# Kernel optimization log

Hardware: AMD Instinct MI355X
Metric: run time of the kernel (lower is better)

Reference implementation:

```python
import jax, jax.numpy as jnp
import numpy as np

B, L, D = 32, 1024, 1024

def setup_inputs() -> dict:
    key = jax.random.key(0)
    k1, k2 = jax.random.split(key)
    x = jax.random.normal(k1, (B, L, D), dtype=jnp.float32)
    x_mask = jax.random.randint(k2, (B, L), 0, 2, dtype=jnp.int32)
    return {"x": x, "x_mask": x_mask}

def reference(x, x_mask):
    # scores: [B, L, L] = x @ x^T
    scores = jnp.einsum('bld,bmd->blm', x, x)
    # zero out the diagonal (the python loop in the original)
    L_ = x.shape[1]
    eye = jnp.eye(L_, dtype=scores.dtype)
    scores = scores * (1.0 - eye)
    # allennlp util.masked_softmax (default, non-memory-efficient form):
    #   a = softmax(scores * mask) * mask; a = a / (a.sum(-1) + 1e-13)
    mask = x_mask[:, None, :].astype(scores.dtype)  # [B, 1, L] broadcast over query dim
    a = jax.nn.softmax(scores * mask, axis=-1) * mask
    alpha = a / (jnp.sum(a, axis=-1, keepdims=True) + 1e-13)
    # matched_seq: [B, L, D]
    return jnp.einsum('blm,bmd->bld', alpha, x)
```

## Files before the change

### kernel.cpp

```cpp
#include <hip/hip_runtime.h>


typedef _Float16 half8 __attribute__((ext_vector_type(8)));
typedef float f32x4 __attribute__((ext_vector_type(4)));

#define L_ 1024
#define D_ 1024

__device__ __forceinline__ half8 cvt8(const float* src) {
  float4 a = *(const float4*)src;
  float4 c = *(const float4*)(src + 4);
  half8 h;
  h[0] = (_Float16)a.x; h[1] = (_Float16)a.y; h[2] = (_Float16)a.z; h[3] = (_Float16)a.w;
  h[4] = (_Float16)c.x; h[5] = (_Float16)c.y; h[6] = (_Float16)c.z; h[7] = (_Float16)c.w;
  return h;
}


__global__ void sam_cvt(const float* __restrict__ x, _Float16* __restrict__ xh) {
  const size_t base = ((size_t)blockIdx.x * 256 + threadIdx.x) * 32;
  const float* src = x + base;
  _Float16* dst = xh + base;
#pragma unroll
  for (int i = 0; i < 4; ++i)
    *(half8*)(dst + i * 8) = cvt8(src + i * 8);
}

__global__ __launch_bounds__(1024, 4) void sam_scores3(
    const _Float16* __restrict__ xh, const int* __restrict__ xmask,
    _Float16* __restrict__ alpha)
{
  const int qblk = blockIdx.x;
  const int b    = blockIdx.y;
  const int tid  = threadIdx.x;
  const int wave = tid >> 6;
  const int lane = tid & 63;
  const int qw   = wave >> 3;
  const int kw   = wave & 7;
  const int l15  = lane & 15;
  const int quad = lane >> 4;

  __shared__ _Float16 Qs[64][72];
  __shared__ union KsAt {
    _Float16 Ks[1024][72];
    _Float16 At[64][1032];
  } KU;
  __shared__ float rmax[8][64];
  __shared__ float rsum[8][64];

  const _Float16* xb = xh + (size_t)b * L_ * D_;
  const int srow = tid >> 3;
  const int scol = (tid & 7) * 8;

  f32x4 acc[2][8];
#pragma unroll
  for (int m = 0; m < 2; ++m)
#pragma unroll
    for (int n = 0; n < 8; ++n)
#pragma unroll
      for (int r = 0; r < 4; ++r) acc[m][n][r] = 0.0f;

  for (int dc = 0; dc < 16; ++dc) {
    if (tid < 512)
      *(half8*)&Qs[srow][scol] =
          *(const half8*)(xb + (size_t)(qblk * 64 + srow) * D_ + dc * 64 + scol);
#pragma unroll
    for (int i = 0; i < 8; ++i)
      *(half8*)&KU.Ks[srow + 128 * i][scol] =
          *(const half8*)(xb + (size_t)(srow + 128 * i) * D_ + dc * 64 + scol);
    __syncthreads();
#pragma unroll
    for (int ks = 0; ks < 2; ++ks) {
      half8 af[2], bf[8];
#pragma unroll
      for (int m = 0; m < 2; ++m)
        af[m] = *(half8*)&Qs[qw * 32 + 16 * m + l15][ks * 32 + quad * 8];
#pragma unroll
      for (int n = 0; n < 8; ++n)
        bf[n] = *(half8*)&KU.Ks[kw * 128 + 16 * n + l15][ks * 32 + quad * 8];
#pragma unroll
      for (int m = 0; m < 2; ++m)
#pragma unroll
        for (int n = 0; n < 8; ++n)
          acc[m][n] = __builtin_amdgcn_mfma_f32_16x16x32_f16(af[m], bf[n], acc[m][n], 0, 0, 0);
    }
    __syncthreads();
  }

  float mkv[8];
#pragma unroll
  for (int n = 0; n < 8; ++n)
    mkv[n] = (float)xmask[b * L_ + kw * 128 + 16 * n + l15];

  float rst[2][4];
#pragma unroll
  for (int m = 0; m < 2; ++m)
#pragma unroll
    for (int r = 0; r < 4; ++r) rst[m][r] = 0.0f;

#pragma unroll
  for (int m = 0; m < 2; ++m)
#pragma unroll
    for (int r = 0; r < 4; ++r) {
      const int gq = qblk * 64 + qw * 32 + 16 * m + quad * 4 + r;
#pragma unroll
      for (int n = 0; n < 8; ++n) {
        const int gk = kw * 128 + 16 * n + l15;
        float v = acc[m][n][r];
        if (gq == gk) v = 0.0f;
        v = (mkv[n] != 0.0f) ? v : 0.0f;
        acc[m][n][r] = v;
        rst[m][r] = fmaxf(rst[m][r], v);
      }
    }
#pragma unroll
  for (int m = 0; m < 2; ++m)
#pragma unroll
    for (int r = 0; r < 4; ++r) {
      float v = rst[m][r];
      v = fmaxf(v, __shfl_xor(v, 1));
      v = fmaxf(v, __shfl_xor(v, 2));
      v = fmaxf(v, __shfl_xor(v, 4));
      v = fmaxf(v, __shfl_xor(v, 8));
      rst[m][r] = v;
    }
  if (l15 == 0) {
#pragma unroll
    for (int m = 0; m < 2; ++m)
#pragma unroll
      for (int r = 0; r < 4; ++r)
        rmax[kw][qw * 32 + 16 * m + quad * 4 + r] = rst[m][r];
  }
  __syncthreads();

  float Mrow[2][4];
#pragma unroll
  for (int m = 0; m < 2; ++m)
#pragma unroll
    for (int r = 0; r < 4; ++r) {
      const int row = qw * 32 + 16 * m + quad * 4 + r;
      float M = fmaxf(fmaxf(rmax[0][row], rmax[1][row]), fmaxf(rmax[2][row], rmax[3][row]));
      M = fmaxf(M, fmaxf(fmaxf(rmax[4][row], rmax[5][row]), fmaxf(rmax[6][row], rmax[7][row])));
      Mrow[m][r] = M;
      rst[m][r] = 0.0f;
    }
#pragma unroll
  for (int m = 0; m < 2; ++m)
#pragma unroll
    for (int r = 0; r < 4; ++r)
#pragma unroll
      for (int n = 0; n < 8; ++n) {
        float w = (mkv[n] != 0.0f) ? __expf(acc[m][n][r] - Mrow[m][r]) : 0.0f;
        acc[m][n][r] = w;
        rst[m][r] += w;
      }
#pragma unroll
  for (int m = 0; m < 2; ++m)
#pragma unroll
    for (int r = 0; r < 4; ++r) {
      float v = rst[m][r];
      v += __shfl_xor(v, 1);
      v += __shfl_xor(v, 2);
      v += __shfl_xor(v, 4);
      v += __shfl_xor(v, 8);
      rst[m][r] = v;
    }
  if (l15 == 0) {
#pragma unroll
    for (int m = 0; m < 2; ++m)
#pragma unroll
      for (int r = 0; r < 4; ++r)
        rsum[kw][qw * 32 + 16 * m + quad * 4 + r] = rst[m][r];
  }
  __syncthreads();

#pragma unroll
  for (int m = 0; m < 2; ++m)
#pragma unroll
    for (int r = 0; r < 4; ++r) {
      const int row = qw * 32 + 16 * m + quad * 4 + r;
      float S = rsum[0][row] + rsum[1][row] + rsum[2][row] + rsum[3][row] +
                rsum[4][row] + rsum[5][row] + rsum[6][row] + rsum[7][row];
      const float inv = 1.0f / (S + 1e-13f);
#pragma unroll
      for (int n = 0; n < 8; ++n)
        KU.At[row][kw * 128 + 16 * n + l15] = (_Float16)(acc[m][n][r] * inv);
    }
  __syncthreads();

  {
    const int orow = tid >> 4;
    const int oc   = (tid & 15) * 8;
    _Float16* gp = alpha + ((size_t)(b * L_ + qblk * 64 + orow)) * L_;
#pragma unroll
    for (int p = 0; p < 8; ++p)
      *(half8*)(gp + oc + p * 128) = *(half8*)&KU.At[orow][oc + p * 128];
  }
}

__global__ __launch_bounds__(512, 3) void sam_pv2(
    const _Float16* __restrict__ xh, const _Float16* __restrict__ alpha,
    float* __restrict__ out)
{
  const int qb   = blockIdx.x >> 1;
  const int dh   = blockIdx.x & 1;
  const int b    = blockIdx.y;
  const int tid  = threadIdx.x;
  const int wave = tid >> 6;
  const int lane = tid & 63;
  const int qw   = wave >> 2;
  const int dw   = wave & 3;
  const int l15  = lane & 15;
  const int quad = lane >> 4;

  __shared__ _Float16 Vs[512][40];
  __shared__ _Float16 As[64][40];

  f32x4 acc[2][8];
#pragma unroll
  for (int m = 0; m < 2; ++m)
#pragma unroll
    for (int n = 0; n < 8; ++n)
#pragma unroll
      for (int r = 0; r < 4; ++r) acc[m][n][r] = 0.0f;

  const int d0 = (tid & 255) * 2;
  const int kh = tid >> 8;

  for (int kc = 0; kc < 32; ++kc) {
    if (tid < 256) {
      const int ar = tid >> 2, ac = tid & 3;
      *(half8*)&As[ar][ac * 8] =
          *(const half8*)(alpha + ((size_t)(b * L_ + qb * 64 + ar)) * L_ + kc * 32 + ac * 8);
    }
    {
      const _Float16* vp = xh + ((size_t)(b * L_ + kc * 32 + kh * 16)) * D_ + dh * 512 + d0;
      half8 a0, a1, c0, c1;
#pragma unroll
      for (int kk = 0; kk < 8; ++kk) {
        union { unsigned int u; _Float16 h[2]; } cv;
        cv.u = *(const unsigned int*)(vp + (size_t)kk * D_);
        a0[kk] = cv.h[0]; c0[kk] = cv.h[1];
      }
#pragma unroll
      for (int kk = 0; kk < 8; ++kk) {
        union { unsigned int u; _Float16 h[2]; } cv;
        cv.u = *(const unsigned int*)(vp + (size_t)(kk + 8) * D_);
        a1[kk] = cv.h[0]; c1[kk] = cv.h[1];
      }
      *(half8*)&Vs[d0    ][kh * 16    ] = a0;
      *(half8*)&Vs[d0    ][kh * 16 + 8] = a1;
      *(half8*)&Vs[d0 + 1][kh * 16    ] = c0;
      *(half8*)&Vs[d0 + 1][kh * 16 + 8] = c1;
    }
    __syncthreads();
    half8 af[2], bf[8];
#pragma unroll
    for (int m = 0; m < 2; ++m)
      af[m] = *(half8*)&As[qw * 32 + 16 * m + l15][quad * 8];
#pragma unroll
    for (int n = 0; n < 8; ++n)
      bf[n] = *(half8*)&Vs[dw * 128 + 16 * n + l15][quad * 8];
#pragma unroll
    for (int m = 0; m < 2; ++m)
#pragma unroll
      for (int n = 0; n < 8; ++n)
        acc[m][n] = __builtin_amdgcn_mfma_f32_16x16x32_f16(af[m], bf[n], acc[m][n], 0, 0, 0);
    __syncthreads();
  }

#pragma unroll
  for (int m = 0; m < 2; ++m)
#pragma unroll
    for (int r = 0; r < 4; ++r) {
      const int gq = qb * 64 + qw * 32 + 16 * m + quad * 4 + r;
      float* op = out + (size_t)(b * L_ + gq) * D_ + dh * 512 + dw * 128;
#pragma unroll
      for (int n = 0; n < 8; ++n) op[16 * n + l15] = acc[m][n][r];
    }
}


__global__ __launch_bounds__(256, 2) void sam_scores_softmax(
    const float* __restrict__ x, const int* __restrict__ xmask,
    float* __restrict__ out)
{
  const int qblk = blockIdx.x;
  const int b    = blockIdx.y;
  const int tid  = threadIdx.x;
  const int wave = tid >> 6;
  const int lane = tid & 63;
  const int qh   = wave >> 1;
  const int kh   = wave & 1;
  const int l15  = lane & 15;
  const int quad = lane >> 4;

  __shared__ _Float16 Qs[128][72];
  __shared__ _Float16 Ks[256][72];
  __shared__ float msk[256];
  __shared__ float tmax[2][128];
  __shared__ float tsum[2][128];
  __shared__ float mrun[128];
  __shared__ float lrun[128];
  __shared__ float mtile[4][128];

  if (tid < 128) { mrun[tid] = 0.0f; lrun[tid] = 0.0f; }

  const float* xb = x + (size_t)b * L_ * D_;

  for (int kt = 0; kt < 4; ++kt) {
    msk[tid] = (float)xmask[b * L_ + kt * 256 + tid];

    f32x4 acc[4][8];
#pragma unroll
    for (int m = 0; m < 4; ++m)
#pragma unroll
      for (int n = 0; n < 8; ++n)
#pragma unroll
        for (int r = 0; r < 4; ++r) acc[m][n][r] = 0.0f;

    for (int dc = 0; dc < 16; ++dc) {
      {
        const int row = tid >> 1, cb = (tid & 1) * 32;
        const float* src = xb + (size_t)(qblk * 128 + row) * D_ + dc * 64 + cb;
#pragma unroll
        for (int i = 0; i < 4; ++i)
          *(half8*)&Qs[row][cb + i * 8] = cvt8(src + i * 8);
      }
      {
        const float* src = xb + (size_t)(kt * 256 + tid) * D_ + dc * 64;
#pragma unroll
        for (int i = 0; i < 8; ++i)
          *(half8*)&Ks[tid][i * 8] = cvt8(src + i * 8);
      }
      __syncthreads();
#pragma unroll
      for (int ks = 0; ks < 2; ++ks) {
        half8 af[4], bf[8];
#pragma unroll
        for (int m = 0; m < 4; ++m)
          af[m] = *(half8*)&Qs[qh * 64 + 16 * m + l15][ks * 32 + quad * 8];
#pragma unroll
        for (int n = 0; n < 8; ++n)
          bf[n] = *(half8*)&Ks[kh * 128 + 16 * n + l15][ks * 32 + quad * 8];
#pragma unroll
        for (int m = 0; m < 4; ++m)
#pragma unroll
          for (int n = 0; n < 8; ++n)
            acc[m][n] = __builtin_amdgcn_mfma_f32_16x16x32_f16(af[m], bf[n], acc[m][n], 0, 0, 0);
      }
      __syncthreads();
    }

    float mkv[8];
#pragma unroll
    for (int n = 0; n < 8; ++n) mkv[n] = msk[kh * 128 + 16 * n + l15];

    float rstat[4][4];
#pragma unroll
    for (int m = 0; m < 4; ++m)
#pragma unroll
      for (int r = 0; r < 4; ++r) rstat[m][r] = 0.0f;

#pragma unroll
    for (int m = 0; m < 4; ++m)
#pragma unroll
      for (int r = 0; r < 4; ++r) {
        const int gq = qblk * 128 + qh * 64 + 16 * m + quad * 4 + r;
#pragma unroll
        for (int n = 0; n < 8; ++n) {
          const int gk = kt * 256 + kh * 128 + 16 * n + l15;
          float v = acc[m][n][r];
          if (gq == gk) v = 0.0f;
          v = (mkv[n] != 0.0f) ? v : 0.0f;
          acc[m][n][r] = v;
          rstat[m][r] = fmaxf(rstat[m][r], v);
        }
      }
#pragma unroll
    for (int m = 0; m < 4; ++m)
#pragma unroll
      for (int r = 0; r < 4; ++r) {
        float v = rstat[m][r];
        v = fmaxf(v, __shfl_xor(v, 1));
        v = fmaxf(v, __shfl_xor(v, 2));
        v = fmaxf(v, __shfl_xor(v, 4));
        v = fmaxf(v, __shfl_xor(v, 8));
        rstat[m][r] = v;
      }
    if (l15 == 0) {
#pragma unroll
      for (int m = 0; m < 4; ++m)
#pragma unroll
        for (int r = 0; r < 4; ++r)
          tmax[kh][qh * 64 + 16 * m + quad * 4 + r] = rstat[m][r];
    }
    __syncthreads();

    float mnew[4][4];
#pragma unroll
    for (int m = 0; m < 4; ++m)
#pragma unroll
      for (int r = 0; r < 4; ++r) {
        const int row = qh * 64 + 16 * m + quad * 4 + r;
        mnew[m][r] = fmaxf(mrun[row], fmaxf(tmax[0][row], tmax[1][row]));
        rstat[m][r] = 0.0f;
      }
#pragma unroll
    for (int m = 0; m < 4; ++m)
#pragma unroll
      for (int r = 0; r < 4; ++r)
#pragma unroll
        for (int n = 0; n < 8; ++n) {
          float w = (mkv[n] != 0.0f) ? __expf(acc[m][n][r] - mnew[m][r]) : 0.0f;
          acc[m][n][r] = w;
          rstat[m][r] += w;
        }
#pragma unroll
    for (int m = 0; m < 4; ++m)
#pragma unroll
      for (int r = 0; r < 4; ++r) {
        float v = rstat[m][r];
        v += __shfl_xor(v, 1);
        v += __shfl_xor(v, 2);
        v += __shfl_xor(v, 4);
        v += __shfl_xor(v, 8);
        rstat[m][r] = v;
      }
    if (l15 == 0) {
#pragma unroll
      for (int m = 0; m < 4; ++m)
#pragma unroll
        for (int r = 0; r < 4; ++r)
          tsum[kh][qh * 64 + 16 * m + quad * 4 + r] = rstat[m][r];
    }
    __syncthreads();

    if (kh == 0 && l15 == 0) {
#pragma unroll
      for (int m = 0; m < 4; ++m)
#pragma unroll
        for (int r = 0; r < 4; ++r) {
          const int row = qh * 64 + 16 * m + quad * 4 + r;
          const float mo = mrun[row];
          const float mn = mnew[m][r];
          lrun[row] = lrun[row] * __expf(mo - mn) + tsum[0][row] + tsum[1][row];
          mrun[row] = mn;
          mtile[kt][row] = mn;
        }
    }
#pragma unroll
    for (int m = 0; m < 4; ++m)
#pragma unroll
      for (int r = 0; r < 4; ++r) {
        const int gq = qblk * 128 + qh * 64 + 16 * m + quad * 4 + r;
        _Float16* wp = (_Float16*)((char*)out + (size_t)(b * L_ + gq) * (D_ * 4));
#pragma unroll
        for (int n = 0; n < 8; ++n)
          wp[kt * 256 + kh * 128 + 16 * n + l15] = (_Float16)acc[m][n][r];
      }
    __syncthreads();
  }

  __threadfence();
  __syncthreads();
  {
    const int row = tid >> 1, hf = tid & 1;
    const int gq = qblk * 128 + row;
    char* rowp = (char*)out + (size_t)(b * L_ + gq) * (D_ * 4);
    const float Mv  = mrun[row];
    const float inv = 1.0f / (lrun[row] + 1e-13f);
    const float sc0 = __expf(mtile[hf * 2    ][row] - Mv) * inv;
    const float sc1 = __expf(mtile[hf * 2 + 1][row] - Mv) * inv;
    for (int i = 0; i < 64; ++i) {
      const int col = hf * 512 + i * 8;
      const float s = (i < 32) ? sc0 : sc1;
      half8 v = *(half8*)(rowp + col * 2);
#pragma unroll
      for (int j = 0; j < 8; ++j) v[j] = (_Float16)((float)v[j] * s);
      *(half8*)(rowp + col * 2) = v;
      *(half8*)(rowp + 2048 + col * 2) = v;
    }
  }
}

__global__ __launch_bounds__(512, 2) void sam_pv(
    const float* __restrict__ x, float* __restrict__ out)
{
  const int q128 = blockIdx.x >> 1;
  const int dh   = blockIdx.x & 1;
  const int b    = blockIdx.y;
  const int tid  = threadIdx.x;
  const int wave = tid >> 6;
  const int lane = tid & 63;
  const int qh   = wave >> 2;
  const int dq   = wave & 3;
  const int l15  = lane & 15;
  const int quad = lane >> 4;

  __shared__ _Float16 Vs[512][40];
  __shared__ _Float16 As[128][40];

  f32x4 acc[4][8];
#pragma unroll
  for (int m = 0; m < 4; ++m)
#pragma unroll
    for (int n = 0; n < 8; ++n)
#pragma unroll
      for (int r = 0; r < 4; ++r) acc[m][n][r] = 0.0f;

  const int arow  = tid >> 2, aoct = tid & 3;
  const int d0    = (tid & 255) * 2;
  const int khalf = tid >> 8;

  for (int kc = 0; kc < 32; ++kc) {
    *(half8*)&As[arow][aoct * 8] =
        *(const half8*)((const char*)out +
                        (size_t)(b * L_ + q128 * 128 + arow) * (D_ * 4) +
                        dh * 2048 + kc * 64 + aoct * 16);
    {
      const float* vs = x + (size_t)(b * L_ + kc * 32 + khalf * 16) * D_ + dh * 512 + d0;
      half8 a0, a1, c0, c1;
#pragma unroll
      for (int kk = 0; kk < 8; ++kk) {
        float2 v = *(const float2*)(vs + (size_t)kk * D_);
        a0[kk] = (_Float16)v.x; c0[kk] = (_Float16)v.y;
      }
#pragma unroll
      for (int kk = 0; kk < 8; ++kk) {
        float2 v = *(const float2*)(vs + (size_t)(kk + 8) * D_);
        a1[kk] = (_Float16)v.x; c1[kk] = (_Float16)v.y;
      }
      *(half8*)&Vs[d0    ][khalf * 16    ] = a0;
      *(half8*)&Vs[d0    ][khalf * 16 + 8] = a1;
      *(half8*)&Vs[d0 + 1][khalf * 16    ] = c0;
      *(half8*)&Vs[d0 + 1][khalf * 16 + 8] = c1;
    }
    __syncthreads();
    half8 af[4], bf[8];
#pragma unroll
    for (int m = 0; m < 4; ++m)
      af[m] = *(half8*)&As[qh * 64 + 16 * m + l15][quad * 8];
#pragma unroll
    for (int n = 0; n < 8; ++n)
      bf[n] = *(half8*)&Vs[dq * 128 + 16 * n + l15][quad * 8];
#pragma unroll
    for (int m = 0; m < 4; ++m)
#pragma unroll
      for (int n = 0; n < 8; ++n)
        acc[m][n] = __builtin_amdgcn_mfma_f32_16x16x32_f16(af[m], bf[n], acc[m][n], 0, 0, 0);
    __syncthreads();
  }

#pragma unroll
  for (int m = 0; m < 4; ++m)
#pragma unroll
    for (int r = 0; r < 4; ++r) {
      const int gq = q128 * 128 + qh * 64 + 16 * m + quad * 4 + r;
      float* op = out + (size_t)(b * L_ + gq) * D_ + dh * 512 + dq * 128;
#pragma unroll
      for (int n = 0; n < 8; ++n) op[16 * n + l15] = acc[m][n][r];
    }
}

extern "C" void kernel_launch(void* const* d_in, const int* in_sizes, int n_in,
                              void* d_out, int out_size, void* d_ws, size_t ws_size,
                              hipStream_t stream) {
  const float* x  = (const float*)d_in[0];
  const int*   xm = (const int*)d_in[1];
  float* out = (float*)d_out;
  (void)in_sizes; (void)n_in; (void)out_size;

  if (ws_size >= (size_t)128 * 1024 * 1024) {
    _Float16* xhp = (_Float16*)d_ws;
    _Float16* alp = (_Float16*)((char*)d_ws + (size_t)64 * 1024 * 1024);
    sam_cvt<<<4096, 256, 0, stream>>>(x, xhp);
    sam_scores3<<<dim3(16, 32), 1024, 0, stream>>>(xhp, xm, alp);
    sam_pv2<<<dim3(32, 32), 512, 0, stream>>>(xhp, alp, out);
  } else {
    sam_scores_softmax<<<dim3(8, 32), 256, 0, stream>>>(x, xm, out);
    sam_pv<<<dim3(16, 32), 512, 0, stream>>>(x, out);
  }
}
```

Measured before the change: 474.5 us.

## Add transposed fp16 copy of x and simple PV kernel with XCD-aware block remap

The conversion kernel now also writes a transposed fp16 copy of x through a shared-memory transpose. A new PV kernel reads that copy so V fragments load contiguously for MFMA without an in-kernel transpose. Both scores and PV kernels remap block IDs so consecutive blocks on the same XCD share a batch, for better L2 reuse. This needs 64MB more workspace and an extra transposed write pass, and the new PV kernel is a simple non-pipelined loop that may give up some of the old kernel's tuning.

```diff
diff --git a/kernel.cpp b/kernel.cpp
--- a/kernel.cpp
+++ b/kernel.cpp
@@ -26,12 +26,57 @@
     *(half8*)(dst + i * 8) = cvt8(src + i * 8);
 }
 
+__global__ __launch_bounds__(256) void sam_cvt2(
+    const float* __restrict__ x, _Float16* __restrict__ xh,
+    _Float16* __restrict__ xhT)
+{
+  const int kt = blockIdx.x >> 4;
+  const int dt = blockIdx.x & 15;
+  const int b  = blockIdx.y;
+  const int tid = threadIdx.x;
+
+  __shared__ float T[64][65];
+
+  const int row = tid >> 2;
+  const int cg  = tid & 3;
+  const float* src = x + ((size_t)(b * L_ + kt * 64 + row)) * D_ + dt * 64 + cg * 16;
+  float4 f0 = ((const float4*)src)[0];
+  float4 f1 = ((const float4*)src)[1];
+  float4 f2 = ((const float4*)src)[2];
+  float4 f3 = ((const float4*)src)[3];
+  half8 h0, h1;
+  h0[0]=(_Float16)f0.x; h0[1]=(_Float16)f0.y; h0[2]=(_Float16)f0.z; h0[3]=(_Float16)f0.w;
+  h0[4]=(_Float16)f1.x; h0[5]=(_Float16)f1.y; h0[6]=(_Float16)f1.z; h0[7]=(_Float16)f1.w;
+  h1[0]=(_Float16)f2.x; h1[1]=(_Float16)f2.y; h1[2]=(_Float16)f2.z; h1[3]=(_Float16)f2.w;
+  h1[4]=(_Float16)f3.x; h1[5]=(_Float16)f3.y; h1[6]=(_Float16)f3.z; h1[7]=(_Float16)f3.w;
+  _Float16* dst = xh + ((size_t)(b * L_ + kt * 64 + row)) * D_ + dt * 64 + cg * 16;
+  *(half8*)dst = h0; *(half8*)(dst + 8) = h1;
+  const int c0 = cg * 16;
+  T[row][c0+ 0]=f0.x; T[row][c0+ 1]=f0.y; T[row][c0+ 2]=f0.z; T[row][c0+ 3]=f0.w;
+  T[row][c0+ 4]=f1.x; T[row][c0+ 5]=f1.y; T[row][c0+ 6]=f1.z; T[row][c0+ 7]=f1.w;
+  T[row][c0+ 8]=f2.x; T[row][c0+ 9]=f2.y; T[row][c0+10]=f2.z; T[row][c0+11]=f2.w;
+  T[row][c0+12]=f3.x; T[row][c0+13]=f3.y; T[row][c0+14]=f3.z; T[row][c0+15]=f3.w;
+  __syncthreads();
+
+  const int dloc = tid >> 2;
+  const int kg   = tid & 3;
+  half8 o0, o1;
+#pragma unroll
+  for (int j = 0; j < 8; ++j) o0[j] = (_Float16)T[kg * 16 + j][dloc];
+#pragma unroll
+  for (int j = 0; j < 8; ++j) o1[j] = (_Float16)T[kg * 16 + 8 + j][dloc];
+  _Float16* tdst = xhT + ((size_t)(b * D_ + dt * 64 + dloc)) * L_ + kt * 64 + kg * 16;
+  *(half8*)tdst = o0; *(half8*)(tdst + 8) = o1;
+}
+
 __global__ __launch_bounds__(1024, 4) void sam_scores3(
     const _Float16* __restrict__ xh, const int* __restrict__ xmask,
     _Float16* __restrict__ alpha)
 {
-  const int qblk = blockIdx.x;
-  const int b    = blockIdx.y;
+  const int id   = blockIdx.y * 16 + blockIdx.x;
+  const int wid  = (id & 7) * 64 + (id >> 3);
+  const int qblk = wid & 15;
+  const int b    = wid >> 4;
   const int tid  = threadIdx.x;
   const int wave = tid >> 6;
   const int lane = tid & 63;
@@ -196,6 +241,78 @@
     for (int p = 0; p < 8; ++p)
       *(half8*)(gp + oc + p * 128) = *(half8*)&KU.At[orow][oc + p * 128];
   }
+}
+
+__global__ __launch_bounds__(512, 3) void sam_pv3(
+    const _Float16* __restrict__ xhT, const _Float16* __restrict__ alpha,
+    float* __restrict__ out)
+{
+  const int id  = blockIdx.y * 32 + blockIdx.x;
+  const int wid = (id & 7) * 128 + (id >> 3);
+  const int b   = wid >> 5;
+  const int rr  = wid & 31;
+  const int qb  = rr >> 1;
+  const int dh  = rr & 1;
+  const int tid  = threadIdx.x;
+  const int wave = tid >> 6;
+  const int lane = tid & 63;
+  const int qw   = wave >> 2;
+  const int dw   = wave & 3;
+  const int l15  = lane & 15;
+  const int quad = lane >> 4;
+
+  __shared__ _Float16 Vs[512][40];
+  __shared__ _Float16 As[64][40];
+
+  f32x4 acc[2][8];
+#pragma unroll
+  for (int m = 0; m < 2; ++m)
+#pragma unroll
+    for (int n = 0; n < 8; ++n)
+#pragma unroll
+      for (int r = 0; r < 4; ++r) acc[m][n][r] = 0.0f;
+
+  const _Float16* xT = xhT + (size_t)b * L_ * D_;
+
+  for (int kc = 0; kc < 32; ++kc) {
+    if (tid < 256) {
+      const int ar = tid >> 2, ac = tid & 3;
+      *(half8*)&As[ar][ac * 8] =
+          *(const half8*)(alpha + ((size_t)(b * L_ + qb * 64 + ar)) * L_ + kc * 32 + ac * 8);
+    }
+#pragma unroll
+    for (int i = 0; i < 4; ++i) {
+      const int c   = tid + 512 * i;
+      const int row = c >> 2;
+      const int cg  = c & 3;
+      *(half8*)&Vs[row][cg * 8] =
+          *(const half8*)(xT + (size_t)(dh * 512 + row) * L_ + kc * 32 + cg * 8);
+    }
+    __syncthreads();
+    half8 af[2], bf[8];
+#pragma unroll
+    for (int m = 0; m < 2; ++m)
+      af[m] = *(half8*)&As[qw * 32 + 16 * m + l15][quad * 8];
+#pragma unroll
+    for (int n = 0; n < 8; ++n)
+      bf[n] = *(half8*)&Vs[dw * 128 + 16 * n + l15][quad * 8];
+#pragma unroll
+    for (int m = 0; m < 2; ++m)
+#pragma unroll
+      for (int n = 0; n < 8; ++n)
+        acc[m][n] = __builtin_amdgcn_mfma_f32_16x16x32_f16(af[m], bf[n], acc[m][n], 0, 0, 0);
+    __syncthreads();
+  }
+
+#pragma unroll
+  for (int m = 0; m < 2; ++m)
+#pragma unroll
+    for (int r = 0; r < 4; ++r) {
+      const int gq = qb * 64 + qw * 32 + 16 * m + quad * 4 + r;
+      float* op = out + (size_t)(b * L_ + gq) * D_ + dh * 512 + dw * 128;
+#pragma unroll
+      for (int n = 0; n < 8; ++n) op[16 * n + l15] = acc[m][n][r];
+    }
 }
 
 __global__ __launch_bounds__(512, 3) void sam_pv2(
@@ -571,7 +688,14 @@
   float* out = (float*)d_out;
   (void)in_sizes; (void)n_in; (void)out_size;
 
-  if (ws_size >= (size_t)128 * 1024 * 1024) {
+  if (ws_size >= (size_t)192 * 1024 * 1024) {
+    _Float16* xhp = (_Float16*)d_ws;
+    _Float16* alp = (_Float16*)((char*)d_ws + (size_t)64 * 1024 * 1024);
+    _Float16* xtp = (_Float16*)((char*)d_ws + (size_t)128 * 1024 * 1024);
+    sam_cvt2<<<dim3(256, 32), 256, 0, stream>>>(x, xhp, xtp);
+    sam_scores3<<<dim3(16, 32), 1024, 0, stream>>>(xhp, xm, alp);
+    sam_pv3<<<dim3(32, 32), 512, 0, stream>>>(xtp, alp, out);
+  } else if (ws_size >= (size_t)128 * 1024 * 1024) {
     _Float16* xhp = (_Float16*)d_ws;
     _Float16* alp = (_Float16*)((char*)d_ws + (size_t)64 * 1024 * 1024);
     sam_cvt<<<4096, 256, 0, stream>>>(x, xhp);
```

After: 551.5 us. 16.2% more time.

## Double-buffer score GEMM tiles via register prefetch with 512-thread blocks

Applied to the files above, without the earlier changes.

Rewrites the scores kernel to use 512 threads (8 waves), each wave covering all 64 query rows against a 128-key slice, which doubles per-wave MFMA accumulators. K and Q tiles are now 32-wide chunks, double-buffered in shared memory and prefetched into registers for the next chunk while the current chunk's MFMAs run. This needs only one barrier per chunk instead of two and is meant to hide global load latency. The cost is more register pressure (acc grows to 4x8 tiles) and twice as many loop iterations with smaller chunks.

```diff
diff --git a/kernel.cpp b/kernel.cpp
--- a/kernel.cpp
+++ b/kernel.cpp
@@ -26,64 +26,84 @@
     *(half8*)(dst + i * 8) = cvt8(src + i * 8);
 }
 
-__global__ __launch_bounds__(1024, 4) void sam_scores3(
+__global__ __launch_bounds__(512, 2) void sam_scores4(
     const _Float16* __restrict__ xh, const int* __restrict__ xmask,
     _Float16* __restrict__ alpha)
 {
   const int qblk = blockIdx.x;
   const int b    = blockIdx.y;
   const int tid  = threadIdx.x;
-  const int wave = tid >> 6;
+  const int kw   = tid >> 6;
   const int lane = tid & 63;
-  const int qw   = wave >> 3;
-  const int kw   = wave & 7;
   const int l15  = lane & 15;
   const int quad = lane >> 4;
 
-  __shared__ _Float16 Qs[64][72];
+  __shared__ _Float16 Qs[2][64][36];
   __shared__ union KsAt {
-    _Float16 Ks[1024][72];
+    _Float16 Ks[2][1024][36];
     _Float16 At[64][1032];
   } KU;
   __shared__ float rmax[8][64];
   __shared__ float rsum[8][64];
 
   const _Float16* xb = xh + (size_t)b * L_ * D_;
-  const int srow = tid >> 3;
-  const int scol = (tid & 7) * 8;
-
-  f32x4 acc[2][8];
-#pragma unroll
-  for (int m = 0; m < 2; ++m)
+  const int krow = tid >> 2;
+  const int kcol = (tid & 3) * 8;
+  const int qrow = tid >> 2;
+  const int qcol = (tid & 3) * 8;
+
+  f32x4 acc[4][8];
+#pragma unroll
+  for (int m = 0; m < 4; ++m)
 #pragma unroll
     for (int n = 0; n < 8; ++n)
 #pragma unroll
       for (int r = 0; r < 4; ++r) acc[m][n][r] = 0.0f;
 
-  for (int dc = 0; dc < 16; ++dc) {
-    if (tid < 512)
-      *(half8*)&Qs[srow][scol] =
-          *(const half8*)(xb + (size_t)(qblk * 64 + srow) * D_ + dc * 64 + scol);
-#pragma unroll
-    for (int i = 0; i < 8; ++i)
-      *(half8*)&KU.Ks[srow + 128 * i][scol] =
-          *(const half8*)(xb + (size_t)(srow + 128 * i) * D_ + dc * 64 + scol);
-    __syncthreads();
-#pragma unroll
-    for (int ks = 0; ks < 2; ++ks) {
-      half8 af[2], bf[8];
-#pragma unroll
-      for (int m = 0; m < 2; ++m)
-        af[m] = *(half8*)&Qs[qw * 32 + 16 * m + l15][ks * 32 + quad * 8];
+  half8 kreg[8];
+  half8 qreg;
+
+#pragma unroll
+  for (int i = 0; i < 8; ++i)
+    kreg[i] = *(const half8*)(xb + (size_t)(krow + 128 * i) * D_ + kcol);
+  if (tid < 256)
+    qreg = *(const half8*)(xb + (size_t)(qblk * 64 + qrow) * D_ + qcol);
+#pragma unroll
+  for (int i = 0; i < 8; ++i)
+    *(half8*)&KU.Ks[0][krow + 128 * i][kcol] = kreg[i];
+  if (tid < 256) *(half8*)&Qs[0][qrow][qcol] = qreg;
+  __syncthreads();
+
+  for (int dc = 0; dc < 32; ++dc) {
+    const int cur = dc & 1;
+    if (dc < 31) {
+      const int c0 = (dc + 1) * 32;
+#pragma unroll
+      for (int i = 0; i < 8; ++i)
+        kreg[i] = *(const half8*)(xb + (size_t)(krow + 128 * i) * D_ + c0 + kcol);
+      if (tid < 256)
+        qreg = *(const half8*)(xb + (size_t)(qblk * 64 + qrow) * D_ + c0 + qcol);
+    }
+    {
+      half8 af[4], bf[8];
+#pragma unroll
+      for (int m = 0; m < 4; ++m)
+        af[m] = *(half8*)&Qs[cur][16 * m + l15][quad * 8];
 #pragma unroll
       for (int n = 0; n < 8; ++n)
-        bf[n] = *(half8*)&KU.Ks[kw * 128 + 16 * n + l15][ks * 32 + quad * 8];
-#pragma unroll
-      for (int m = 0; m < 2; ++m)
+        bf[n] = *(half8*)&KU.Ks[cur][kw * 128 + 16 * n + l15][quad * 8];
+#pragma unroll
+      for (int m = 0; m < 4; ++m)
 #pragma unroll
         for (int n = 0; n < 8; ++n)
           acc[m][n] = __builtin_amdgcn_mfma_f32_16x16x32_f16(af[m], bf[n], acc[m][n], 0, 0, 0);
     }
+    if (dc < 31) {
+#pragma unroll
+      for (int i = 0; i < 8; ++i)
+        *(half8*)&KU.Ks[cur ^ 1][krow + 128 * i][kcol] = kreg[i];
+      if (tid < 256) *(half8*)&Qs[cur ^ 1][qrow][qcol] = qreg;
+    }
     __syncthreads();
   }
 
@@ -92,17 +112,17 @@
   for (int n = 0; n < 8; ++n)
     mkv[n] = (float)xmask[b * L_ + kw * 128 + 16 * n + l15];
 
-  float rst[2][4];
-#pragma unroll
-  for (int m = 0; m < 2; ++m)
+  float rst[4][4];
+#pragma unroll
+  for (int m = 0; m < 4; ++m)
 #pragma unroll
     for (int r = 0; r < 4; ++r) rst[m][r] = 0.0f;
 
 #pragma unroll
-  for (int m = 0; m < 2; ++m)
+  for (int m = 0; m < 4; ++m)
 #pragma unroll
     for (int r = 0; r < 4; ++r) {
-      const int gq = qblk * 64 + qw * 32 + 16 * m + quad * 4 + r;
+      const int gq = qblk * 64 + 16 * m + quad * 4 + r;
 #pragma unroll
       for (int n = 0; n < 8; ++n) {
         const int gk = kw * 128 + 16 * n + l15;
@@ -114,7 +134,7 @@
       }
     }
 #pragma unroll
-  for (int m = 0; m < 2; ++m)
+  for (int m = 0; m < 4; ++m)
 #pragma unroll
     for (int r = 0; r < 4; ++r) {
       float v = rst[m][r];
@@ -126,26 +146,26 @@
     }
   if (l15 == 0) {
 #pragma unroll
-    for (int m = 0; m < 2; ++m)
+    for (int m = 0; m < 4; ++m)
 #pragma unroll
       for (int r = 0; r < 4; ++r)
-        rmax[kw][qw * 32 + 16 * m + quad * 4 + r] = rst[m][r];
+        rmax[kw][16 * m + quad * 4 + r] = rst[m][r];
   }
   __syncthreads();
 
-  float Mrow[2][4];
-#pragma unroll
-  for (int m = 0; m < 2; ++m)
+  float Mrow[4][4];
+#pragma unroll
+  for (int m = 0; m < 4; ++m)
 #pragma unroll
     for (int r = 0; r < 4; ++r) {
-      const int row = qw * 32 + 16 * m + quad * 4 + r;
+      const int row = 16 * m + quad * 4 + r;
       float M = fmaxf(fmaxf(rmax[0][row], rmax[1][row]), fmaxf(rmax[2][row], rmax[3][row]));
       M = fmaxf(M, fmaxf(fmaxf(rmax[4][row], rmax[5][row]), fmaxf(rmax[6][row], rmax[7][row])));
       Mrow[m][r] = M;
       rst[m][r] = 0.0f;
     }
 #pragma unroll
-  for (int m = 0; m < 2; ++m)
+  for (int m = 0; m < 4; ++m)
 #pragma unroll
     for (int r = 0; r < 4; ++r)
 #pragma unroll
@@ -155,7 +175,7 @@
         rst[m][r] += w;
       }
 #pragma unroll
-  for (int m = 0; m < 2; ++m)
+  for (int m = 0; m < 4; ++m)
 #pragma unroll
     for (int r = 0; r < 4; ++r) {
       float v = rst[m][r];
@@ -167,18 +187,18 @@
     }
   if (l15 == 0) {
 #pragma unroll
-    for (int m = 0; m < 2; ++m)
+    for (int m = 0; m < 4; ++m)
 #pragma unroll
       for (int r = 0; r < 4; ++r)
-        rsum[kw][qw * 32 + 16 * m + quad * 4 + r] = rst[m][r];
+        rsum[kw][16 * m + quad * 4 + r] = rst[m][r];
   }
   __syncthreads();
 
 #pragma unroll
-  for (int m = 0; m < 2; ++m)
+  for (int m = 0; m < 4; ++m)
 #pragma unroll
     for (int r = 0; r < 4; ++r) {
-      const int row = qw * 32 + 16 * m + quad * 4 + r;
+      const int row = 16 * m + quad * 4 + r;
       float S = rsum[0][row] + rsum[1][row] + rsum[2][row] + rsum[3][row] +
                 rsum[4][row] + rsum[5][row] + rsum[6][row] + rsum[7][row];
       const float inv = 1.0f / (S + 1e-13f);
@@ -189,12 +209,12 @@
   __syncthreads();
 
   {
-    const int orow = tid >> 4;
-    const int oc   = (tid & 15) * 8;
+    const int orow = tid >> 3;
+    const int oc   = (tid & 7) * 8;
     _Float16* gp = alpha + ((size_t)(b * L_ + qblk * 64 + orow)) * L_;
 #pragma unroll
-    for (int p = 0; p < 8; ++p)
-      *(half8*)(gp + oc + p * 128) = *(half8*)&KU.At[orow][oc + p * 128];
+    for (int p = 0; p < 16; ++p)
+      *(half8*)(gp + oc + p * 64) = *(half8*)&KU.At[orow][oc + p * 64];
   }
 }
 
@@ -575,7 +595,7 @@
     _Float16* xhp = (_Float16*)d_ws;
     _Float16* alp = (_Float16*)((char*)d_ws + (size_t)64 * 1024 * 1024);
     sam_cvt<<<4096, 256, 0, stream>>>(x, xhp);
-    sam_scores3<<<dim3(16, 32), 1024, 0, stream>>>(xhp, xm, alp);
+    sam_scores4<<<dim3(16, 32), 512, 0, stream>>>(xhp, xm, alp);
     sam_pv2<<<dim3(32, 32), 512, 0, stream>>>(xhp, alp, out);
   } else {
     sam_scores_softmax<<<dim3(8, 32), 256, 0, stream>>>(x, xm, out);
```

Measured after the change: 625.7 us. 31.9% more time.
